# Kernel tuning notes

Hardware: AMD Instinct MI355X
Metric: run time of the kernel (lower is better)

## Reference

```python
import jax, jax.numpy as jnp
import numpy as np

N = 8192      # active sparse voxels
C = 768       # model_channels
H = 12        # heads
DH = 64       # head dim
NB = 12       # blocks
WS = 8        # window size
RES = 64      # voxel grid resolution
NG = 32       # gaussians per voxel
OUT_CH = 448  # 96+96+96+128+32


def _radical_inverse(base, n):
    inv, f = 0.0, 1.0 / base
    while n > 0:
        inv += f * (n % base)
        n //= base
        f /= base
    return inv


def _hammersley(num):
    return np.array([[i / num, _radical_inverse(2, i), _radical_inverse(3, i)]
                     for i in range(num)], dtype=np.float32)


def _windows(coords, shift):
    # swin partition: window id of each voxel after shifting coords
    wc = (coords.astype(np.int64) + shift) // WS
    G = (RES + shift) // WS + 1
    wid = (wc[:, 0] * G + wc[:, 1]) * G + wc[:, 2]
    uniq, vwin, counts = np.unique(wid, return_inverse=True, return_counts=True)
    nw, cap, n = len(uniq), int(counts.max()), len(wid)
    order = np.argsort(wid, kind='stable')
    starts = np.concatenate([[0], np.cumsum(counts)[:-1]])
    slot_sorted = np.arange(n) - starts[vwin[order]]
    vslot = np.empty(n, dtype=np.int64)
    vslot[order] = slot_sorted
    idx = np.full((nw, cap), n, dtype=np.int32)  # n = padding row
    idx[vwin, vslot] = np.arange(n)
    mask = idx < n
    return (jnp.asarray(idx), jnp.asarray(mask),
            jnp.asarray(vwin.astype(np.int32)), jnp.asarray(vslot.astype(np.int32)))


def setup_inputs() -> dict:
    rng = np.random.RandomState(0)
    coords = rng.randint(0, RES, size=(N, 3)).astype(np.int32)
    feats = rng.randn(N, 8).astype(np.float32)
    idx0, mask0, vwin0, vslot0 = _windows(coords, 0)          # even blocks
    idx1, mask1, vwin1, vslot1 = _windows(coords, WS // 2)    # odd blocks (shifted)
    s = 0.02
    def w(*shape):
        return jnp.asarray((rng.randn(*shape) * s).astype(np.float32))
    perturb = _hammersley(NG) * 2.0 - 1.0
    perturb = np.arctanh(perturb / 1.5).astype(np.float32)  # voxel_size=1.5
    return dict(
        feats=jnp.asarray(feats), coords=jnp.asarray(coords),
        in_w=w(8, C), in_b=jnp.zeros((C,), jnp.float32),
        qkv_w=w(NB, C, 3 * C), qkv_b=jnp.zeros((NB, 3 * C), jnp.float32),
        proj_w=w(NB, C, C), proj_b=jnp.zeros((NB, C), jnp.float32),
        mlp_w1=w(NB, C, 4 * C), mlp_b1=jnp.zeros((NB, 4 * C), jnp.float32),
        mlp_w2=w(NB, 4 * C, C), mlp_b2=jnp.zeros((NB, C), jnp.float32),
        out_w=w(C, OUT_CH), out_b=jnp.zeros((OUT_CH,), jnp.float32),
        perturb=jnp.asarray(perturb),
        idx0=idx0, mask0=mask0, vwin0=vwin0, vslot0=vslot0,
        idx1=idx1, mask1=mask1, vwin1=vwin1, vslot1=vslot1,
    )


def _ln(x, eps):
    mu = jnp.mean(x, -1, keepdims=True)
    xc = x - mu
    var = jnp.mean(xc * xc, -1, keepdims=True)
    return xc * jax.lax.rsqrt(var + eps)


def _pos_embed(coords):
    freq_dim = C // 3 // 2  # 128
    freqs = 1.0 / (10000.0 ** (jnp.arange(freq_dim, dtype=jnp.float32) / freq_dim))
    phase = coords.astype(jnp.float32)[..., None] * freqs          # [N,3,128]
    emb = jnp.concatenate([jnp.sin(phase), jnp.cos(phase)], -1)    # [N,3,256]
    return emb.reshape(coords.shape[0], C)


def _win_attn(q, k, v, idx, mask):
    zpad = jnp.zeros((1,) + q.shape[1:], q.dtype)
    qw = jnp.concatenate([q, zpad], 0)[idx]   # [nw,cap,H,DH]
    kw = jnp.concatenate([k, zpad], 0)[idx]
    vw = jnp.concatenate([v, zpad], 0)[idx]
    scores = jnp.einsum('wihd,wjhd->whij', qw, kw) / np.float32(np.sqrt(DH))
    scores = jnp.where(mask[:, None, None, :], scores, jnp.float32(-1e9))
    attn = jax.nn.softmax(scores, axis=-1)
    return jnp.einsum('whij,wjhd->wihd', attn, vw)   # [nw,cap,H,DH]


def _forward(feats, coords, in_w, in_b, qkv_w, qkv_b, proj_w, proj_b,
             mlp_w1, mlp_b1, mlp_w2, mlp_b2, out_w, out_b, perturb,
             idx0, mask0, vwin0, vslot0, idx1, mask1, vwin1, vslot1):
    cfgs = [(idx0, mask0, vwin0, vslot0), (idx1, mask1, vwin1, vslot1)]
    n = feats.shape[0]
    h = feats @ in_w + in_b + _pos_embed(coords)
    for i in range(NB):
        idx, mask, vwin, vslot = cfgs[i % 2]
        qkv = (_ln(h, 1e-6) @ qkv_w[i] + qkv_b[i]).reshape(n, 3, H, DH)
        ow = _win_attn(qkv[:, 0], qkv[:, 1], qkv[:, 2], idx, mask)
        o = ow[vwin, vslot].reshape(n, C)
        h = h + (o @ proj_w[i] + proj_b[i])
        hid = jax.nn.gelu(_ln(h, 1e-6) @ mlp_w1[i] + mlp_b1[i], approximate=False)
        h = h + (hid @ mlp_w2[i] + mlp_b2[i])
    out = _ln(h, 1e-5) @ out_w + out_b   # F.layer_norm default eps
    # to_representation
    xyz = (coords.astype(jnp.float32) + 0.5) / RES                   # [N,3]
    off = out[:, :96].reshape(n, NG, 3)                               # lr=1.0
    off = jnp.tanh(off + perturb) / RES * 0.5 * 1.5                   # voxel_size=1.5
    g_xyz = (xyz[:, None, :] + off).reshape(n * NG, 3)
    g_dc = out[:, 96:192].reshape(n * NG, 3)
    g_scal = out[:, 192:288].reshape(n * NG, 3)
    g_rot = out[:, 288:416].reshape(n * NG, 4) * 0.1                  # lr=0.1
    g_opa = out[:, 416:448].reshape(n * NG, 1)
    return jnp.concatenate([g_xyz, g_dc, g_scal, g_rot, g_opa], -1)   # [N*32,14]


def reference(feats, coords, in_w, in_b, qkv_w, qkv_b, proj_w, proj_b,
              mlp_w1, mlp_b1, mlp_w2, mlp_b2, out_w, out_b, perturb,
              idx0, mask0, vwin0, vslot0, idx1, mask1, vwin1, vslot1):
    return _forward(feats, coords, in_w, in_b, qkv_w, qkv_b, proj_w, proj_b,
                    mlp_w1, mlp_b1, mlp_w2, mlp_b2, out_w, out_b, perturb,
                    idx0, mask0, vwin0, vslot0, idx1, mask1, vwin1, vslot1)
```

## Files before the change

### kernel.cpp

```cpp
#include <hip/hip_runtime.h>
#include <math.h>

#define NVOX 8192
#define CCH 768
#define NH 12
#define DH 64
#define NBLK 12
#define NG 32
#define OUT_CH 448
#define OUT_PAD 512
#define CAP 48
#define APITCH 72

typedef __attribute__((ext_vector_type(8))) short v8s;
typedef __attribute__((ext_vector_type(4))) float v4f;

__device__ __forceinline__ unsigned short f2bf(float f) {
  unsigned u = __builtin_bit_cast(unsigned, f);
  u += 0x7fffu + ((u >> 16) & 1u);
  return (unsigned short)(u >> 16);
}
__device__ __forceinline__ float bf2f(unsigned short b) {
  return __builtin_bit_cast(float, (unsigned)b << 16);
}

__device__ __forceinline__ void async16(const void* g, void* l) {
  __builtin_amdgcn_global_load_lds(
      (const __attribute__((address_space(1))) unsigned int*)g,
      (__attribute__((address_space(3))) unsigned int*)l, 16, 0, 0);
}

__global__ __launch_bounds__(256) void cap_kernel(const int* __restrict__ a,
                                                  const int* __restrict__ b,
                                                  int n, int* __restrict__ caps) {
  __shared__ int s0[256], s1[256];
  int m0 = 0, m1 = 0;
  for (int i = threadIdx.x; i < n; i += 256) {
    m0 = max(m0, a[i]);
    m1 = max(m1, b[i]);
  }
  s0[threadIdx.x] = m0;
  s1[threadIdx.x] = m1;
  __syncthreads();
  for (int st = 128; st > 0; st >>= 1) {
    if (threadIdx.x < st) {
      s0[threadIdx.x] = max(s0[threadIdx.x], s0[threadIdx.x + st]);
      s1[threadIdx.x] = max(s1[threadIdx.x], s1[threadIdx.x + st]);
    }
    __syncthreads();
  }
  if (threadIdx.x == 0) {
    caps[0] = s0[0] + 1;
    caps[1] = s1[0] + 1;
  }
}

__global__ __launch_bounds__(256) void embed_kernel(const float* __restrict__ feats,
                                                    const int* __restrict__ coords,
                                                    const float* __restrict__ in_w,
                                                    const float* __restrict__ in_b,
                                                    float* __restrict__ h) {
  int id = blockIdx.x * 256 + threadIdx.x;
  if (id >= NVOX * CCH) return;
  int n = id / CCH, c = id - n * CCH;
  float acc = in_b[c];
#pragma unroll
  for (int k = 0; k < 8; ++k) acc += feats[n * 8 + k] * in_w[k * CCH + c];
  int axis = c / 256;
  int r = c - axis * 256;
  int f = r & 127;
  float freq = __expf(-(float)f * (9.210340371976184f / 128.0f));
  float phase = (float)coords[n * 3 + axis] * freq;
  acc += (r < 128) ? __sinf(phase) : __cosf(phase);
  h[id] = acc;
}

__global__ __launch_bounds__(256) void ln_kernel(const float* __restrict__ x,
                                                 unsigned short* __restrict__ y,
                                                 float eps) {
  int row = blockIdx.x;
  const float* xr = x + (size_t)row * CCH;
  float v[3];
  float s = 0.f, s2 = 0.f;
#pragma unroll
  for (int j = 0; j < 3; ++j) {
    v[j] = xr[threadIdx.x + j * 256];
    s += v[j];
    s2 += v[j] * v[j];
  }
#pragma unroll
  for (int off = 32; off >= 1; off >>= 1) {
    s += __shfl_xor(s, off, 64);
    s2 += __shfl_xor(s2, off, 64);
  }
  __shared__ float ss[4], ss2[4];
  int wave = threadIdx.x >> 6, lane = threadIdx.x & 63;
  if (lane == 0) { ss[wave] = s; ss2[wave] = s2; }
  __syncthreads();
  s = ss[0] + ss[1] + ss[2] + ss[3];
  s2 = ss2[0] + ss2[1] + ss2[2] + ss2[3];
  float mu = s * (1.0f / CCH);
  float var = s2 * (1.0f / CCH) - mu * mu;
  float rr = rsqrtf(var + eps);
  unsigned short* yr = y + (size_t)row * CCH;
#pragma unroll
  for (int j = 0; j < 3; ++j) yr[threadIdx.x + j * 256] = f2bf((v[j] - mu) * rr);
}

__device__ __forceinline__ void wconv_tile(const float* __restrict__ W,
                                           unsigned short* __restrict__ Wt,
                                           int K, int Nsrc, int nt, int kt,
                                           float (*t)[65]) {
  int n0 = nt * 64, k0 = kt * 64;
  for (int e = threadIdx.x; e < 4096; e += 256) {
    int r = e >> 6, c = e & 63;
    int n = n0 + c;
    t[r][c] = (n < Nsrc) ? W[(size_t)(k0 + r) * Nsrc + n] : 0.f;
  }
  __syncthreads();
  for (int e = threadIdx.x; e < 4096; e += 256) {
    int rn = e >> 6, ck = e & 63;
    Wt[(size_t)(n0 + rn) * K + k0 + ck] = f2bf(t[ck][rn]);
  }
}

__global__ __launch_bounds__(256) void wconvert(const float* __restrict__ W,
                                                unsigned short* __restrict__ Wt,
                                                int K, int Nsrc) {
  __shared__ float t[64][65];
  wconv_tile(W, Wt, K, Nsrc, blockIdx.x, blockIdx.y, t);
}

__global__ __launch_bounds__(256) void wconvert4(const float* __restrict__ W0,
                                                 const float* __restrict__ W1,
                                                 const float* __restrict__ W2,
                                                 const float* __restrict__ W3,
                                                 unsigned short* __restrict__ D0,
                                                 unsigned short* __restrict__ D1,
                                                 unsigned short* __restrict__ D2,
                                                 unsigned short* __restrict__ D3) {
  __shared__ float t[64][65];
  int b = blockIdx.x;
  if (b < 432) {
    wconv_tile(W0, D0, 768, 2304, b / 12, b % 12, t);
  } else if (b < 576) {
    b -= 432;
    wconv_tile(W1, D1, 768, 768, b / 12, b % 12, t);
  } else if (b < 1152) {
    b -= 576;
    wconv_tile(W2, D2, 768, 3072, b / 12, b % 12, t);
  } else {
    b -= 1152;
    wconv_tile(W3, D3, 3072, 768, b / 48, b % 48, t);
  }
}

__device__ __forceinline__ float gelu_exact(float x) {
  return 0.5f * x * (1.0f + erff(x * 0.70710678118654752f));
}

template <int ACT, int RES, int OUTBF>
__global__ __launch_bounds__(256) void gemm_mfma(const unsigned short* __restrict__ A,
                                                 const unsigned short* __restrict__ Bt,
                                                 const float* __restrict__ bias, int Nbias,
                                                 float* __restrict__ outf,
                                                 unsigned short* __restrict__ outb,
                                                 int Nn, int K) {
  __shared__ __align__(16) unsigned short As[2][128 * 32];
  __shared__ __align__(16) unsigned short Bs[2][128 * 32];
  const int tid = threadIdx.x;
  const int lane = tid & 63, w = tid >> 6;

  int bx = blockIdx.x, by = blockIdx.y;
  {
    const int gx = gridDim.x, gy = gridDim.y;
    const int nwg = gx * gy;
    const int id = by * gx + bx;
    const int q = nwg >> 3, r = nwg & 7;
    const int xc = id & 7, off = id >> 3;
    const int nid = (xc < r ? xc * (q + 1) : r * (q + 1) + (xc - r) * q) + off;
    bx = nid % gx;
    by = nid / gx;
  }
  const int row0 = by * 128, col0 = bx * 128;
  const int wm = (w >> 1) * 64, wn = (w & 1) * 64;
  const int fm = lane & 15, fq = lane >> 4;

  const int c0 = w * 64 + lane;
  const int c1 = c0 + 256;
  const unsigned short* gA0 = A + (size_t)(row0 + (c0 >> 2)) * K + (c0 & 3) * 8;
  const unsigned short* gA1 = A + (size_t)(row0 + (c1 >> 2)) * K + (c1 & 3) * 8;
  const unsigned short* gB0 = Bt + (size_t)(col0 + (c0 >> 2)) * K + (c0 & 3) * 8;
  const unsigned short* gB1 = Bt + (size_t)(col0 + (c1 >> 2)) * K + (c1 & 3) * 8;
  const int oL0 = w * 512;
  const int oL1 = w * 512 + 2048;

  v4f acc[4][4];
#pragma unroll
  for (int i = 0; i < 4; ++i)
#pragma unroll
    for (int j = 0; j < 4; ++j) acc[i][j] = (v4f){0.f, 0.f, 0.f, 0.f};

  async16(gA0, As[0] + oL0);
  async16(gA1, As[0] + oL1);
  async16(gB0, Bs[0] + oL0);
  async16(gB1, Bs[0] + oL1);
  __syncthreads();

  int cur = 0;
  for (int k0 = 32; k0 < K; k0 += 32) {
    const int nxt = cur ^ 1;
    async16(gA0 + k0, As[nxt] + oL0);
    async16(gA1 + k0, As[nxt] + oL1);
    async16(gB0 + k0, Bs[nxt] + oL0);
    async16(gB1 + k0, Bs[nxt] + oL1);
    v8s af[4], bfv[4];
#pragma unroll
    for (int i = 0; i < 4; ++i)
      af[i] = *(const v8s*)(As[cur] + (wm + i * 16 + fm) * 32 + fq * 8);
#pragma unroll
    for (int j = 0; j < 4; ++j)
      bfv[j] = *(const v8s*)(Bs[cur] + (wn + j * 16 + fm) * 32 + fq * 8);
#pragma unroll
    for (int i = 0; i < 4; ++i)
#pragma unroll
      for (int j = 0; j < 4; ++j)
        acc[i][j] = __builtin_amdgcn_mfma_f32_16x16x32_bf16(af[i], bfv[j], acc[i][j], 0, 0, 0);
    __syncthreads();
    cur = nxt;
  }
  {
    v8s af[4], bfv[4];
#pragma unroll
    for (int i = 0; i < 4; ++i)
      af[i] = *(const v8s*)(As[cur] + (wm + i * 16 + fm) * 32 + fq * 8);
#pragma unroll
    for (int j = 0; j < 4; ++j)
      bfv[j] = *(const v8s*)(Bs[cur] + (wn + j * 16 + fm) * 32 + fq * 8);
#pragma unroll
    for (int i = 0; i < 4; ++i)
#pragma unroll
      for (int j = 0; j < 4; ++j)
        acc[i][j] = __builtin_amdgcn_mfma_f32_16x16x32_bf16(af[i], bfv[j], acc[i][j], 0, 0, 0);
  }

#pragma unroll
  for (int i = 0; i < 4; ++i) {
    int row = row0 + wm + i * 16 + fq * 4;
#pragma unroll
    for (int j = 0; j < 4; ++j) {
      int col = col0 + wn + j * 16 + fm;
      float b = (col < Nbias) ? bias[col] : 0.f;
#pragma unroll
      for (int r = 0; r < 4; ++r) {
        float v = acc[i][j][r] + b;
        if (ACT == 1) v = gelu_exact(v);
        size_t o = (size_t)(row + r) * Nn + col;
        if (RES) {
          outf[o] += v;
        } else if (OUTBF) {
          outb[o] = f2bf(v);
        } else {
          outf[o] = v;
        }
      }
    }
  }
}

__global__ __launch_bounds__(64) void attn_kernel(const unsigned short* __restrict__ qkv,
                                                  const int* __restrict__ idx,
                                                  const int* __restrict__ capPtr,
                                                  int total,
                                                  unsigned short* __restrict__ attn_out) {
  __shared__ __align__(16) unsigned short QP[CAP * APITCH];
  __shared__ __align__(16) unsigned short Ks[CAP * APITCH];
  __shared__ __align__(16) unsigned short Vt[64 * APITCH];
  __shared__ int vox_lds[64];
  const int cap = *capPtr;
  if (cap > CAP) return;
  const int nw = total / cap;
  const int tasks = nw * NH;
  const int lane = threadIdx.x;
  const int fm = lane & 15, fq = lane >> 4;
  const v8s z8 = {0, 0, 0, 0, 0, 0, 0, 0};

  for (int task = blockIdx.x; task < tasks; task += gridDim.x) {
    const int w = task / NH, hh = task - w * NH;
    int vox_i = NVOX;
    if (lane < cap) vox_i = idx[w * cap + lane];
    vox_lds[lane] = vox_i;
    __syncthreads();

#pragma unroll
    for (int it = 0; it < 6; ++it) {
      int id = it * 64 + lane;
      int j = id >> 3, c = id & 7;
      int vj = vox_lds[j];
      v8s q8 = z8, k8 = z8;
      if (vj < NVOX) {
        const unsigned short* base = qkv + (size_t)vj * (3 * CCH) + hh * DH + c * 8;
        q8 = *(const v8s*)(base);
        k8 = *(const v8s*)(base + CCH);
      }
      *(v8s*)(QP + j * APITCH + c * 8) = q8;
      *(v8s*)(Ks + j * APITCH + c * 8) = k8;
    }
#pragma unroll 4
    for (int j = 0; j < CAP; ++j) {
      int vj = vox_lds[j];
      unsigned short vv = 0;
      if (vj < NVOX) vv = qkv[(size_t)vj * (3 * CCH) + 2 * CCH + hh * DH + lane];
      Vt[lane * APITCH + j] = vv;
    }
#pragma unroll
    for (int j = CAP; j < 64; ++j) Vt[lane * APITCH + j] = 0;
    __syncthreads();

    v4f s_acc[3][3];
#pragma unroll
    for (int mi = 0; mi < 3; ++mi)
#pragma unroll
      for (int jt = 0; jt < 3; ++jt) s_acc[mi][jt] = (v4f){0.f, 0.f, 0.f, 0.f};
#pragma unroll
    for (int ks = 0; ks < 2; ++ks) {
      v8s qf[3], kf[3];
#pragma unroll
      for (int mi = 0; mi < 3; ++mi)
        qf[mi] = *(const v8s*)(QP + (mi * 16 + fm) * APITCH + ks * 32 + fq * 8);
#pragma unroll
      for (int jt = 0; jt < 3; ++jt)
        kf[jt] = *(const v8s*)(Ks + (jt * 16 + fm) * APITCH + ks * 32 + fq * 8);
#pragma unroll
      for (int mi = 0; mi < 3; ++mi)
#pragma unroll
        for (int jt = 0; jt < 3; ++jt)
          s_acc[mi][jt] = __builtin_amdgcn_mfma_f32_16x16x32_bf16(qf[mi], kf[jt], s_acc[mi][jt], 0, 0, 0);
    }
    __syncthreads();

    bool va0 = (fm < cap) && (vox_lds[fm] < NVOX);
    bool va1 = (16 + fm < cap) && (vox_lds[16 + fm] < NVOX);
    bool va2 = (32 + fm < cap) && (vox_lds[32 + fm] < NVOX);
#pragma unroll
    for (int mi = 0; mi < 3; ++mi) {
#pragma unroll
      for (int r = 0; r < 4; ++r) {
        float e0 = va0 ? __expf(s_acc[mi][0][r] * 0.125f) : 0.f;
        float e1 = va1 ? __expf(s_acc[mi][1][r] * 0.125f) : 0.f;
        float e2 = va2 ? __expf(s_acc[mi][2][r] * 0.125f) : 0.f;
        float den = e0 + e1 + e2;
        den += __shfl_xor(den, 1, 64);
        den += __shfl_xor(den, 2, 64);
        den += __shfl_xor(den, 4, 64);
        den += __shfl_xor(den, 8, 64);
        float rden = (den > 0.f) ? 1.0f / den : 0.f;
        int row = mi * 16 + fq * 4 + r;
        QP[row * APITCH + fm] = f2bf(e0 * rden);
        QP[row * APITCH + 16 + fm] = f2bf(e1 * rden);
        QP[row * APITCH + 32 + fm] = f2bf(e2 * rden);
      }
    }
    if (lane < CAP) {
      *(v8s*)(QP + lane * APITCH + 48) = z8;
      *(v8s*)(QP + lane * APITCH + 56) = z8;
    }
    __syncthreads();

    v4f o_acc[3][4];
#pragma unroll
    for (int mi = 0; mi < 3; ++mi)
#pragma unroll
      for (int nt = 0; nt < 4; ++nt) o_acc[mi][nt] = (v4f){0.f, 0.f, 0.f, 0.f};
#pragma unroll
    for (int ks = 0; ks < 2; ++ks) {
      v8s pf[3], vf[4];
#pragma unroll
      for (int mi = 0; mi < 3; ++mi)
        pf[mi] = *(const v8s*)(QP + (mi * 16 + fm) * APITCH + ks * 32 + fq * 8);
#pragma unroll
      for (int nt = 0; nt < 4; ++nt)
        vf[nt] = *(const v8s*)(Vt + (nt * 16 + fm) * APITCH + ks * 32 + fq * 8);
#pragma unroll
      for (int mi = 0; mi < 3; ++mi)
#pragma unroll
        for (int nt = 0; nt < 4; ++nt)
          o_acc[mi][nt] = __builtin_amdgcn_mfma_f32_16x16x32_bf16(pf[mi], vf[nt], o_acc[mi][nt], 0, 0, 0);
    }

#pragma unroll
    for (int mi = 0; mi < 3; ++mi) {
#pragma unroll
      for (int r = 0; r < 4; ++r) {
        int i = mi * 16 + fq * 4 + r;
        int vox = vox_lds[i];
        if (i < cap && vox < NVOX) {
          unsigned short* ob = attn_out + (size_t)vox * CCH + hh * DH + fm;
#pragma unroll
          for (int nt = 0; nt < 4; ++nt) ob[nt * 16] = f2bf(o_acc[mi][nt][r]);
        }
      }
    }
    __syncthreads();
  }
}

__global__ __launch_bounds__(256) void decode_kernel(const float* __restrict__ outpad,
                                                     const int* __restrict__ coords,
                                                     const float* __restrict__ perturb,
                                                     float* __restrict__ out) {
  __shared__ float row[OUT_CH];
  const int n = blockIdx.x;
  const float* src = outpad + (size_t)n * OUT_PAD;
  for (int e = threadIdx.x; e < OUT_CH; e += 256) row[e] = src[e];
  __syncthreads();
  float* o = out + (size_t)n * OUT_CH;
  for (int e = threadIdx.x; e < OUT_CH; e += 256) {
    int g = e / 14, j = e - g * 14;
    float v;
    if (j < 3) {
      float xyz = ((float)coords[n * 3 + j] + 0.5f) * (1.0f / 64.0f);
      v = xyz + tanhf(row[g * 3 + j] + perturb[g * 3 + j]) * (0.75f / 64.0f);
    } else if (j < 6) {
      v = row[96 + g * 3 + (j - 3)];
    } else if (j < 9) {
      v = row[192 + g * 3 + (j - 6)];
    } else if (j < 13) {
      v = row[288 + g * 4 + (j - 9)] * 0.1f;
    } else {
      v = row[416 + g];
    }
    o[e] = v;
  }
}

extern "C" void kernel_launch(void* const* d_in, const int* in_sizes, int n_in,
                              void* d_out, int out_size, void* d_ws, size_t ws_size,
                              hipStream_t stream) {
  const float* feats = (const float*)d_in[0];
  const int* coords = (const int*)d_in[1];
  const float* in_w = (const float*)d_in[2];
  const float* in_b = (const float*)d_in[3];
  const float* qkv_w = (const float*)d_in[4];
  const float* qkv_b = (const float*)d_in[5];
  const float* proj_w = (const float*)d_in[6];
  const float* proj_b = (const float*)d_in[7];
  const float* mlp_w1 = (const float*)d_in[8];
  const float* mlp_b1 = (const float*)d_in[9];
  const float* mlp_w2 = (const float*)d_in[10];
  const float* mlp_b2 = (const float*)d_in[11];
  const float* out_w = (const float*)d_in[12];
  const float* out_b = (const float*)d_in[13];
  const float* perturb = (const float*)d_in[14];
  const int* idx0 = (const int*)d_in[15];
  const int* vslot0 = (const int*)d_in[18];
  const int* idx1 = (const int*)d_in[19];
  const int* vslot1 = (const int*)d_in[22];
  const int total0 = in_sizes[15];
  const int total1 = in_sizes[19];

  char* p = (char*)d_ws;
  int* caps = (int*)p;
  float* h = (float*)(p + 256);
  unsigned short* abuf = (unsigned short*)(p + 256 + 25165824);
  unsigned short* big = (unsigned short*)(p + 256 + 37748736);
  unsigned short* wst = (unsigned short*)(p + 256 + 88080384);
  float* outpad = (float*)(p + 256 + 102236160);
  const size_t OQ = 0;
  const size_t OP = (size_t)768 * 2304;
  const size_t OM1 = OP + (size_t)768 * 768;
  const size_t OM2 = OM1 + (size_t)768 * 3072;

  cap_kernel<<<1, 256, 0, stream>>>(vslot0, vslot1, NVOX, caps);
  embed_kernel<<<(NVOX * CCH + 255) / 256, 256, 0, stream>>>(feats, coords, in_w, in_b, h);

  for (int i = 0; i < NBLK; ++i) {
    const int* idx = (i & 1) ? idx1 : idx0;
    const int* capP = (i & 1) ? caps + 1 : caps;
    const int total = (i & 1) ? total1 : total0;

    wconvert4<<<1728, 256, 0, stream>>>(
        qkv_w + (size_t)i * 768 * 2304, proj_w + (size_t)i * 768 * 768,
        mlp_w1 + (size_t)i * 768 * 3072, mlp_w2 + (size_t)i * 3072 * 768,
        wst + OQ, wst + OP, wst + OM1, wst + OM2);

    ln_kernel<<<NVOX, 256, 0, stream>>>(h, abuf, 1e-6f);
    gemm_mfma<0, 0, 1><<<dim3(18, 64), 256, 0, stream>>>(
        abuf, wst + OQ, qkv_b + (size_t)i * 2304, 2304, nullptr, big, 2304, 768);
    attn_kernel<<<4096, 64, 0, stream>>>(big, idx, capP, total, abuf);
    gemm_mfma<0, 1, 0><<<dim3(6, 64), 256, 0, stream>>>(
        abuf, wst + OP, proj_b + (size_t)i * 768, 768, h, nullptr, 768, 768);
    ln_kernel<<<NVOX, 256, 0, stream>>>(h, abuf, 1e-6f);
    gemm_mfma<1, 0, 1><<<dim3(24, 64), 256, 0, stream>>>(
        abuf, wst + OM1, mlp_b1 + (size_t)i * 3072, 3072, nullptr, big, 3072, 768);
    gemm_mfma<0, 1, 0><<<dim3(6, 64), 256, 0, stream>>>(
        big, wst + OM2, mlp_b2 + (size_t)i * 768, 768, h, nullptr, 768, 3072);
  }

  ln_kernel<<<NVOX, 256, 0, stream>>>(h, abuf, 1e-5f);
  wconvert<<<dim3(8, 12), 256, 0, stream>>>(out_w, wst + OQ, 768, OUT_CH);
  gemm_mfma<0, 0, 0><<<dim3(4, 64), 256, 0, stream>>>(
      abuf, wst + OQ, out_b, OUT_CH, outpad, nullptr, OUT_PAD, 768);
  decode_kernel<<<NVOX, 256, 0, stream>>>(outpad, coords, perturb, (float*)d_out);
}
```

Measured before the change: 4.400 ms.

## Triple-buffer GEMM LDS loads and XOR-swizzle tiles to avoid bank conflicts

Replaces the double-buffered K loop of the MFMA GEMM with a three-stage ring buffer. Two tiles of async global-to-LDS loads stay in flight, managed with explicit vmcnt waits and barriers. It also applies an XOR swizzle to the 16-byte chunk position within each LDS row, on both the global load side and the fragment read side, to cut LDS bank conflicts. The cost is more LDS per block, which may lower occupancy. It also does redundant dummy loads at the tail, and correctness relies on the hand-set vmcnt(8) matching the number of outstanding loads.

```diff
diff --git a/kernel.cpp b/kernel.cpp
--- a/kernel.cpp
+++ b/kernel.cpp
@@ -11,6 +11,7 @@
 #define OUT_PAD 512
 #define CAP 48
 #define APITCH 72
+#define PIPE 3
 
 typedef __attribute__((ext_vector_type(8))) short v8s;
 typedef __attribute__((ext_vector_type(4))) float v4f;
@@ -166,8 +167,8 @@
                                                  float* __restrict__ outf,
                                                  unsigned short* __restrict__ outb,
                                                  int Nn, int K) {
-  __shared__ __align__(16) unsigned short As[2][128 * 32];
-  __shared__ __align__(16) unsigned short Bs[2][128 * 32];
+  __shared__ __align__(16) unsigned short As[PIPE][128 * 32];
+  __shared__ __align__(16) unsigned short Bs[PIPE][128 * 32];
   const int tid = threadIdx.x;
   const int lane = tid & 63, w = tid >> 6;
 
@@ -188,12 +189,15 @@
 
   const int c0 = w * 64 + lane;
   const int c1 = c0 + 256;
-  const unsigned short* gA0 = A + (size_t)(row0 + (c0 >> 2)) * K + (c0 & 3) * 8;
-  const unsigned short* gA1 = A + (size_t)(row0 + (c1 >> 2)) * K + (c1 & 3) * 8;
-  const unsigned short* gB0 = Bt + (size_t)(col0 + (c0 >> 2)) * K + (c0 & 3) * 8;
-  const unsigned short* gB1 = Bt + (size_t)(col0 + (c1 >> 2)) * K + (c1 & 3) * 8;
+  const int r0s = c0 >> 2, ch0 = (c0 & 3) ^ (r0s & 3);
+  const int r1s = c1 >> 2, ch1 = (c1 & 3) ^ (r1s & 3);
+  const unsigned short* gA0 = A + (size_t)(row0 + r0s) * K + ch0 * 8;
+  const unsigned short* gA1 = A + (size_t)(row0 + r1s) * K + ch1 * 8;
+  const unsigned short* gB0 = Bt + (size_t)(col0 + r0s) * K + ch0 * 8;
+  const unsigned short* gB1 = Bt + (size_t)(col0 + r1s) * K + ch1 * 8;
   const int oL0 = w * 512;
   const int oL1 = w * 512 + 2048;
+  const int xo = ((fq ^ (fm & 3)) * 8);
 
   v4f acc[4][4];
 #pragma unroll
@@ -201,47 +205,46 @@
 #pragma unroll
     for (int j = 0; j < 4; ++j) acc[i][j] = (v4f){0.f, 0.f, 0.f, 0.f};
 
-  async16(gA0, As[0] + oL0);
-  async16(gA1, As[0] + oL1);
-  async16(gB0, Bs[0] + oL0);
-  async16(gB1, Bs[0] + oL1);
-  __syncthreads();
-
-  int cur = 0;
-  for (int k0 = 32; k0 < K; k0 += 32) {
-    const int nxt = cur ^ 1;
-    async16(gA0 + k0, As[nxt] + oL0);
-    async16(gA1 + k0, As[nxt] + oL1);
-    async16(gB0 + k0, Bs[nxt] + oL0);
-    async16(gB1 + k0, Bs[nxt] + oL1);
+  const int NT = K >> 5;
+#pragma unroll
+  for (int t = 0; t < PIPE; ++t) {
+    const int k0 = t * 32;
+    async16(gA0 + k0, (unsigned short*)As + t * 4096 + oL0);
+    async16(gA1 + k0, (unsigned short*)As + t * 4096 + oL1);
+    async16(gB0 + k0, (unsigned short*)Bs + t * 4096 + oL0);
+    async16(gB1 + k0, (unsigned short*)Bs + t * 4096 + oL1);
+  }
+
+  int buf = 0;
+  int kpf = PIPE * 32;
+  for (int t = 0; t < NT; ++t) {
+    unsigned short* Ab = (unsigned short*)As + buf * 4096;
+    unsigned short* Bb = (unsigned short*)Bs + buf * 4096;
+    asm volatile("s_waitcnt vmcnt(8)" ::: "memory");
+    __builtin_amdgcn_s_barrier();
     v8s af[4], bfv[4];
 #pragma unroll
     for (int i = 0; i < 4; ++i)
-      af[i] = *(const v8s*)(As[cur] + (wm + i * 16 + fm) * 32 + fq * 8);
+      af[i] = *(const v8s*)(Ab + (wm + i * 16 + fm) * 32 + xo);
 #pragma unroll
     for (int j = 0; j < 4; ++j)
-      bfv[j] = *(const v8s*)(Bs[cur] + (wn + j * 16 + fm) * 32 + fq * 8);
+      bfv[j] = *(const v8s*)(Bb + (wn + j * 16 + fm) * 32 + xo);
+    asm volatile("s_waitcnt lgkmcnt(0)" ::: "memory");
+    __builtin_amdgcn_s_barrier();
+    {
+      const int kq = (kpf < K) ? kpf : (kpf - PIPE * 32);
+      async16(gA0 + kq, Ab + oL0);
+      async16(gA1 + kq, Ab + oL1);
+      async16(gB0 + kq, Bb + oL0);
+      async16(gB1 + kq, Bb + oL1);
+    }
 #pragma unroll
     for (int i = 0; i < 4; ++i)
 #pragma unroll
       for (int j = 0; j < 4; ++j)
         acc[i][j] = __builtin_amdgcn_mfma_f32_16x16x32_bf16(af[i], bfv[j], acc[i][j], 0, 0, 0);
-    __syncthreads();
-    cur = nxt;
-  }
-  {
-    v8s af[4], bfv[4];
-#pragma unroll
-    for (int i = 0; i < 4; ++i)
-      af[i] = *(const v8s*)(As[cur] + (wm + i * 16 + fm) * 32 + fq * 8);
-#pragma unroll
-    for (int j = 0; j < 4; ++j)
-      bfv[j] = *(const v8s*)(Bs[cur] + (wn + j * 16 + fm) * 32 + fq * 8);
-#pragma unroll
-    for (int i = 0; i < 4; ++i)
-#pragma unroll
-      for (int j = 0; j < 4; ++j)
-        acc[i][j] = __builtin_amdgcn_mfma_f32_16x16x32_bf16(af[i], bfv[j], acc[i][j], 0, 0, 0);
+    kpf += 32;
+    buf = (buf == PIPE - 1) ? 0 : buf + 1;
   }
 
 #pragma unroll
```

Result: faster. 4.135 ms (-6.0%).
